# Kernel optimization log

Measured on AMD Instinct MI355X. Metric: run time of the kernel, lower is better.

## Reference

```python
import jax, jax.numpy as jnp
import numpy as np

H = 12           # num_heads
D_MODEL = 768
SCALE = (D_MODEL // H) ** -0.5  # qk_scale default: head_dim**-0.5


def _attn_mask(q, k, v, mask):
    # sim: (b, i, j); mask broadcast over query dim (mask.unsqueeze(1) in torch)
    sim = jnp.einsum('bid,bjd->bij', q, k) + mask[:, None, :]
    a = jax.nn.softmax(sim, axis=-1)
    return jnp.einsum('bij,bjd->bid', a, v)


def setup_inputs() -> dict:
    key = jax.random.key(0)
    k0, k1, k2, k3 = jax.random.split(key, 4)
    B, F, n, D = 16, 8, 196, 768
    N = 1 + F * n  # cls + frames*patches = 1569
    x = jax.random.normal(k0, (B, N, D), jnp.float32)
    x_mask = jax.random.normal(k1, (B, N), jnp.float32)  # additive attention mask
    Wqkv = jax.random.normal(k2, (3 * D, D), jnp.float32) * (D ** -0.5)
    Wproj = jax.random.normal(k3, (D, D), jnp.float32) * (D ** -0.5)
    bproj = jnp.zeros((D,), jnp.float32)
    return {"x": x, "x_mask": x_mask, "Wqkv": Wqkv, "Wproj": Wproj,
            "bproj": bproj, "f": F}


def reference(x, x_mask, Wqkv, Wproj, bproj, f):
    B, N, D = x.shape
    h = H
    d = D // h
    # qkv projection (qkv_bias=False), split into q,k,v
    qkv = x @ Wqkv.T                       # (B, N, 3D)
    q, k, v = jnp.split(qkv, 3, axis=-1)

    def to_heads(t):  # 'b n (h d) -> (b h) n d'
        return t.reshape(B, N, h, d).transpose(0, 2, 1, 3).reshape(B * h, N, d)

    q, k, v = map(to_heads, (q, k, v))
    mask = jnp.repeat(x_mask, h, axis=0)   # repeat_interleave over heads: (B*h, N)

    q = q * SCALE
    cls_q, q_ = q[:, :1], q[:, 1:]
    cls_k, k_ = k[:, :1], k[:, 1:]
    cls_v, v_ = v[:, :1], v[:, 1:]
    cls_mask, mask_ = mask[:, :1], mask[:, 1:]

    # cls token attends to everything
    cls_out = _attn_mask(cls_q, k, v, mask)            # (B*h, 1, d)

    # spatial attention: 'b (f n) d -> (b f) n d'
    n = (N - 1) // f
    q_ = q_.reshape(B * h * f, n, d)
    k_ = k_.reshape(B * h * f, n, d)
    v_ = v_.reshape(B * h * f, n, d)
    mask_ = mask_.reshape(B * h * f, n)

    # prepend cls k/v/mask to every frame group (r = f)
    cls_k = jnp.repeat(cls_k, f, axis=0)               # (B*h*f, 1, d)
    cls_v = jnp.repeat(cls_v, f, axis=0)
    cls_m = jnp.repeat(cls_mask, f, axis=0)            # (B*h*f, 1)
    k_ = jnp.concatenate([cls_k, k_], axis=1)          # (B*h*f, n+1, d)
    v_ = jnp.concatenate([cls_v, v_], axis=1)
    m2 = jnp.concatenate([cls_m, mask_], axis=1)       # (B*h*f, n+1)

    out = _attn_mask(q_, k_, v_, m2)                   # (B*h*f, n, d)
    out = out.reshape(B * h, f * n, d)                 # '(b f) n d -> b (f n) d'
    out = jnp.concatenate([cls_out, out], axis=1)      # (B*h, N, d)
    out = out.reshape(B, h, N, d).transpose(0, 2, 1, 3).reshape(B, N, D)
    return out @ Wproj.T + bproj
```

## Files before the change

### kernel.cpp

```cpp
#include <hip/hip_runtime.h>
#include <hip/hip_bf16.h>
#include <stdint.h>

#define Hh 12
#define Dm 768
#define Bb 16
#define Nt 1569
#define Ff 8
#define NC 196
#define BH 192
#define Mr 25104
#define CPW 224
#define VTW (8*CPW)
#define PLD 232
#define CLD 132

typedef __attribute__((ext_vector_type(8))) short bf16x8;
typedef __attribute__((ext_vector_type(4))) float f32x4;

typedef const __attribute__((address_space(1))) uint32_t guint;
typedef __attribute__((address_space(3))) uint32_t luint;

static __device__ __forceinline__ float bf2f(unsigned short u) {
  union { unsigned int i; float f; } v; v.i = ((unsigned int)u) << 16; return v.f;
}
static __device__ __forceinline__ unsigned short f2bf(float f) {
  __hip_bfloat16 h = __float2bfloat16(f);
  return __builtin_bit_cast(unsigned short, h);
}

__global__ void cast3_k(const float4* __restrict__ s0, ushort4* __restrict__ d0, int n0,
                        const float4* __restrict__ s1, ushort4* __restrict__ d1, int n1,
                        const float4* __restrict__ s2, ushort4* __restrict__ d2, int n2) {
  int nTot = n0 + n1 + n2;
  for (int i = blockIdx.x * blockDim.x + threadIdx.x; i < nTot; i += gridDim.x * blockDim.x) {
    const float4* s; ushort4* d; int off;
    if (i < n0) { s = s0; d = d0; off = i; }
    else if (i < n0 + n1) { s = s1; d = d1; off = i - n0; }
    else { s = s2; d = d2; off = i - n0 - n1; }
    float4 f = s[off];
    ushort4 u;
    u.x = f2bf(f.x); u.y = f2bf(f.y); u.z = f2bf(f.z); u.w = f2bf(f.w);
    d[off] = u;
  }
}

template<int MODE>
__global__ __launch_bounds__(256) void gemm_k(
    const __hip_bfloat16* __restrict__ A,
    const __hip_bfloat16* __restrict__ W,
    int M, int K,
    __hip_bfloat16* __restrict__ qh, __hip_bfloat16* __restrict__ kh,
    __hip_bfloat16* __restrict__ vT, __hip_bfloat16* __restrict__ vcls,
    const float* __restrict__ bias, float* __restrict__ outp)
{
  __shared__ __align__(16) unsigned short shmem[128 * CLD];
  unsigned short* ls0 = shmem;
  unsigned short* ls1 = shmem + 4096;
  unsigned short* ls2 = shmem + 8192;
  unsigned short* ls3 = shmem + 12288;

  const int tid = threadIdx.x;
  const int lane = tid & 63, wid = tid >> 6;
  const int waveM = wid >> 1, waveN = wid & 1;

  const int gridN = gridDim.x;
  const int nwg = gridDim.x * gridDim.y;
  int bid = blockIdx.y * gridN + blockIdx.x;
  int q8 = nwg >> 3, r8 = nwg & 7;
  int xcd = bid & 7, lid = bid >> 3;
  int swz = (xcd < r8 ? xcd * (q8 + 1) : r8 * (q8 + 1) + (xcd - r8) * q8) + lid;
  const int mBase = (swz / gridN) * 128, nBase = (swz % gridN) * 128;

  const int l15 = lane & 15, lg = lane >> 4;
  f32x4 acc[4][4] = {};
  const int nkt = K >> 6;
  for (int kt = 0; kt < nkt; ++kt) {
#pragma unroll
    for (int s = 0; s < 2; ++s) {
      int seg = s * 256 + tid;
      int row = seg >> 2, ks = seg & 3;
      int arow = mBase + row; if (arow >= M) arow = M - 1;
      int brow = nBase + row;
      const __hip_bfloat16* ap = A + (size_t)arow * K + kt * 64 + ks * 8;
      const __hip_bfloat16* wp = W + (size_t)brow * K + kt * 64 + ks * 8;
      __builtin_amdgcn_global_load_lds((guint*)ap,        (luint*)&ls0[seg * 8], 16, 0, 0);
      __builtin_amdgcn_global_load_lds((guint*)wp,        (luint*)&ls1[seg * 8], 16, 0, 0);
      __builtin_amdgcn_global_load_lds((guint*)(ap + 32), (luint*)&ls2[seg * 8], 16, 0, 0);
      __builtin_amdgcn_global_load_lds((guint*)(wp + 32), (luint*)&ls3[seg * 8], 16, 0, 0);
    }
    __syncthreads();
    bf16x8 aF[4], bF[4], aG[4], bG[4];
#pragma unroll
    for (int i = 0; i < 4; ++i) {
      int ro = (waveM * 64 + i * 16 + l15) * 32 + lg * 8;
      int co = (waveN * 64 + i * 16 + l15) * 32 + lg * 8;
      aF[i] = *reinterpret_cast<const bf16x8*>(&ls0[ro]);
      bF[i] = *reinterpret_cast<const bf16x8*>(&ls1[co]);
      aG[i] = *reinterpret_cast<const bf16x8*>(&ls2[ro]);
      bG[i] = *reinterpret_cast<const bf16x8*>(&ls3[co]);
    }
#pragma unroll
    for (int mi = 0; mi < 4; ++mi)
#pragma unroll
      for (int ni = 0; ni < 4; ++ni) {
        acc[mi][ni] = __builtin_amdgcn_mfma_f32_16x16x32_bf16(aF[mi], bF[ni], acc[mi][ni], 0, 0, 0);
        acc[mi][ni] = __builtin_amdgcn_mfma_f32_16x16x32_bf16(aG[mi], bG[ni], acc[mi][ni], 0, 0, 0);
      }
    __syncthreads();
  }

  if (MODE == 1) {
    const bool fullM = (mBase + 128 <= M);
#pragma unroll
    for (int mi = 0; mi < 4; ++mi)
#pragma unroll
      for (int ni = 0; ni < 4; ++ni)
#pragma unroll
        for (int r = 0; r < 4; ++r) {
          int grow = mBase + waveM * 64 + mi * 16 + lg * 4 + r;
          if (!fullM && grow >= M) continue;
          int gcol = nBase + waveN * 64 + ni * 16 + l15;
          outp[(size_t)grow * Dm + gcol] = acc[mi][ni][r] + bias[gcol];
        }
    return;
  }

  const int which = nBase / Dm;
  const int headBase = (nBase - which * Dm) >> 6;
  const float scl = (which == 0) ? 0.125f : 1.f;
  const bool fullM = (mBase + 128 <= M);

  if (fullM) {
    if (which < 2) {
#pragma unroll
      for (int mi = 0; mi < 4; ++mi)
#pragma unroll
        for (int ni = 0; ni < 4; ++ni)
#pragma unroll
          for (int r = 0; r < 4; ++r)
            shmem[(waveM * 64 + mi * 16 + lg * 4 + r) * CLD + (waveN * 64 + ni * 16 + l15)]
                = f2bf(acc[mi][ni][r] * scl);
      __syncthreads();
      __hip_bfloat16* dst = (which == 0) ? qh : kh;
      int row = tid >> 1, h = tid & 1;
      int grow = mBase + row;
      int b = grow / Nt, i = grow - b * Nt;
      const uint2* sp = reinterpret_cast<const uint2*>(&shmem[row * CLD + h * 64]);
      uint2* dp = reinterpret_cast<uint2*>(
          dst + ((size_t)(b * Hh + headBase + h) * Nt + i) * 64);
#pragma unroll
      for (int j = 0; j < 16; ++j) dp[j] = sp[j];
    } else {
#pragma unroll
      for (int mi = 0; mi < 4; ++mi)
#pragma unroll
        for (int ni = 0; ni < 4; ++ni)
#pragma unroll
          for (int r = 0; r < 4; ++r)
            shmem[(waveN * 64 + ni * 16 + l15) * CLD + (waveM * 64 + mi * 16 + lg * 4 + r)]
                = f2bf(acc[mi][ni][r]);
      __syncthreads();
      int lc = tid & 127, rhalf = tid >> 7;
      int h = lc >> 6, dc = lc & 63;
      int head = headBase + h;
#pragma unroll
      for (int g = 0; g < 8; ++g) {
        int row0 = rhalf * 64 + g * 8;
        int grow0 = mBase + row0;
        int b = grow0 / Nt, i0 = grow0 - b * Nt;
        const unsigned short* sp = &shmem[lc * CLD + row0];
        if (i0 >= 1 && i0 + 8 <= Nt) {
          int j0 = i0 - 1, cc = j0 / NC, key = j0 - cc * NC;
          if (key + 8 <= NC) {
            int bh = b * Hh + head;
            __hip_bfloat16* p = vT + ((size_t)bh * 64 + dc) * VTW + cc * CPW + key;
            if ((key & 1) == 0) {
              const unsigned int* s4 = reinterpret_cast<const unsigned int*>(sp);
              unsigned int* d4 = reinterpret_cast<unsigned int*>(p);
              d4[0] = s4[0]; d4[1] = s4[1]; d4[2] = s4[2]; d4[3] = s4[3];
            } else {
#pragma unroll
              for (int j = 0; j < 8; ++j)
                p[j] = __builtin_bit_cast(__hip_bfloat16, sp[j]);
            }
            continue;
          }
        }
#pragma unroll
        for (int j = 0; j < 8; ++j) {
          int grow = grow0 + j;
          int bb = grow / Nt, ii = grow - bb * Nt;
          int bh2 = bb * Hh + head;
          unsigned short val = sp[j];
          if (ii == 0) {
            vcls[bh2 * 64 + dc] = __builtin_bit_cast(__hip_bfloat16, val);
          } else {
            int jj = ii - 1, cc2 = jj / NC, k2 = jj - cc2 * NC;
            vT[((size_t)bh2 * 64 + dc) * VTW + cc2 * CPW + k2]
                = __builtin_bit_cast(__hip_bfloat16, val);
          }
        }
      }
    }
  } else {
#pragma unroll
    for (int mi = 0; mi < 4; ++mi)
#pragma unroll
      for (int ni = 0; ni < 4; ++ni)
#pragma unroll
        for (int r = 0; r < 4; ++r) {
          int grow = mBase + waveM * 64 + mi * 16 + lg * 4 + r;
          if (grow >= M) continue;
          int gcol = nBase + waveN * 64 + ni * 16 + l15;
          float v = acc[mi][ni][r];
          int b = grow / Nt, i = grow - b * Nt;
          int hcol = gcol - which * Dm;
          int head = hcol >> 6, dc = hcol & 63;
          int bh = b * Hh + head;
          if (which == 0) {
            qh[((size_t)bh * Nt + i) * 64 + dc] = __float2bfloat16(v * 0.125f);
          } else if (which == 1) {
            kh[((size_t)bh * Nt + i) * 64 + dc] = __float2bfloat16(v);
          } else {
            if (i == 0) vcls[bh * 64 + dc] = __float2bfloat16(v);
            else {
              int j = i - 1; int cc = j / NC, key = j - cc * NC;
              vT[((size_t)bh * 64 + dc) * VTW + cc * CPW + key] = __float2bfloat16(v);
            }
          }
        }
  }
}

__global__ __launch_bounds__(512, 2) void attn_k(
    const __hip_bfloat16* __restrict__ qh, const __hip_bfloat16* __restrict__ kh,
    const __hip_bfloat16* __restrict__ vT, const __hip_bfloat16* __restrict__ vcls,
    const float* __restrict__ x_mask, __hip_bfloat16* __restrict__ ao)
{
  __shared__ __align__(16) char smem[118784];

  const int bidx = blockIdx.x;
  const int tid = threadIdx.x;

  if (bidx < BH) {
    float* sS = reinterpret_cast<float*>(smem);
    float* qv = reinterpret_cast<float*>(smem + 6400);
    float* red = reinterpret_cast<float*>(smem + 6656);
    const int bh = bidx, b = bh / Hh, head = bh - b * Hh;
    if (tid < 64) qv[tid] = __bfloat162float(qh[((size_t)bh * Nt) * 64 + tid]);
    __syncthreads();
    float lmax = -1e30f;
    for (int j = tid; j < Nt; j += 512) {
      const __hip_bfloat16* kr = kh + ((size_t)bh * Nt + j) * 64;
      float dot = 0.f;
#pragma unroll
      for (int d0 = 0; d0 < 64; d0 += 8) {
        bf16x8 kv = *reinterpret_cast<const bf16x8*>(kr + d0);
#pragma unroll
        for (int i = 0; i < 8; ++i) dot += qv[d0 + i] * bf2f((unsigned short)kv[i]);
      }
      float s = dot + x_mask[b * Nt + j];
      sS[j] = s;
      lmax = fmaxf(lmax, s);
    }
    red[tid] = lmax; __syncthreads();
    for (int off = 256; off > 0; off >>= 1) {
      if (tid < off) red[tid] = fmaxf(red[tid], red[tid + off]);
      __syncthreads();
    }
    float m = red[0]; __syncthreads();
    float lsum = 0.f;
    for (int j = tid; j < Nt; j += 512) { float e = __expf(sS[j] - m); sS[j] = e; lsum += e; }
    red[tid] = lsum; __syncthreads();
    for (int off = 256; off > 0; off >>= 1) {
      if (tid < off) red[tid] += red[tid + off];
      __syncthreads();
    }
    float rden = 1.f / red[0]; __syncthreads();
    int dc = tid & 63, part = tid >> 6;
    float partial = 0.f;
    if (part == 0) partial = sS[0] * __bfloat162float(vcls[bh * 64 + dc]);
    {
      int base = 1 + part * NC;
      const __hip_bfloat16* vc2 = vT + ((size_t)bh * 64 + dc) * VTW + part * CPW;
      int key = 0;
      for (; key + 8 <= NC; key += 8) {
        bf16x8 vv = *reinterpret_cast<const bf16x8*>(vc2 + key);
#pragma unroll
        for (int i = 0; i < 8; ++i)
          partial += sS[base + key + i] * bf2f((unsigned short)vv[i]);
      }
      for (; key < NC; ++key)
        partial += sS[base + key] * __bfloat162float(vc2[key]);
    }
    red[tid] = partial; __syncthreads();
    if (tid < 64) {
      float o = 0.f;
#pragma unroll
      for (int k = 0; k < 8; ++k) o += red[tid + 64 * k];
      ao[((size_t)b * Nt) * Dm + head * 64 + dc] = __float2bfloat16(o * rden);
    }
    return;
  }

  __hip_bfloat16* ldsK = reinterpret_cast<__hip_bfloat16*>(smem);
  __hip_bfloat16* ldsV = reinterpret_cast<__hip_bfloat16*>(smem + 26624);
  __hip_bfloat16* ldsP = reinterpret_cast<__hip_bfloat16*>(smem + 59392);

  const int g = bidx - BH;
  const int bh = g >> 3, c = g & 7;
  const int b = bh / Hh, head = bh - b * Hh;
  const int lane = tid & 63, wid = tid >> 6;
  const int l15 = lane & 15, lg = lane >> 4;

  const int kbase = 1 + c * NC;

#pragma unroll
  for (int it = 0; it < 4; ++it) {
    int idx = it * 512 + tid;
    if (idx < 1664) {
      int row = idx >> 3, c16 = idx & 7;
      int token = kbase + row; if (token > Nt - 1) token = Nt - 1;
      __builtin_amdgcn_global_load_lds(
          (guint*)(kh + ((size_t)bh * Nt + token) * 64 + ((c16 ^ (row & 7)) * 8)),
          (luint*)&ldsK[idx * 8], 16, 0, 0);
    }
  }
#pragma unroll
  for (int it = 0; it < 4; ++it) {
    int idx = it * 512 + tid;
    if (idx < 1792) {
      int dc = idx / 28, u = idx - dc * 28;
      uint4 v = *reinterpret_cast<const uint4*>(
          vT + ((size_t)bh * 64 + dc) * VTW + c * CPW + u * 8);
      *reinterpret_cast<uint4*>(&ldsV[dc * 256 + ((u ^ (dc & 7)) * 8)]) = v;
    }
  }
  __syncthreads();

  __hip_bfloat16* myP = ldsP + wid * (16 * PLD);

  const __hip_bfloat16* kc = kh + (size_t)bh * Nt * 64;
  bf16x8 ck0 = *reinterpret_cast<const bf16x8*>(kc + lg * 8);
  bf16x8 ck1 = *reinterpret_cast<const bf16x8*>(kc + 32 + lg * 8);
  const float maskCls = x_mask[b * Nt];

  for (int rt = wid; rt < 13; rt += 8) {
    int qlrow = rt * 16 + l15;
    int qtok = 1 + c * NC + qlrow; if (qtok > Nt - 1) qtok = Nt - 1;
    const __hip_bfloat16* qp = qh + ((size_t)bh * Nt + qtok) * 64;
    bf16x8 aQ0 = *reinterpret_cast<const bf16x8*>(qp + lg * 8);
    bf16x8 aQ1 = *reinterpret_cast<const bf16x8*>(qp + 32 + lg * 8);

    float pc0 = 0.f;
#pragma unroll
    for (int i = 0; i < 8; ++i)
      pc0 += bf2f((unsigned short)aQ0[i]) * bf2f((unsigned short)ck0[i])
           + bf2f((unsigned short)aQ1[i]) * bf2f((unsigned short)ck1[i]);
    pc0 += __shfl_xor(pc0, 16);
    pc0 += __shfl_xor(pc0, 32);
    pc0 += maskCls;

    f32x4 S[13];
    float mv[13];
#define LD_MM(i) { \
    int row = (i) * 16 + l15; \
    bf16x8 kb0 = *reinterpret_cast<const bf16x8*>(&ldsK[row * 64 + ((lg ^ (l15 & 7)) * 8)]); \
    bf16x8 kb1 = *reinterpret_cast<const bf16x8*>(&ldsK[row * 64 + (((4 + lg) ^ (l15 & 7)) * 8)]); \
    mv[i] = (row < NC) ? x_mask[b * Nt + kbase + row] : -1e30f; \
    f32x4 sa = {}; \
    sa = __builtin_amdgcn_mfma_f32_16x16x32_bf16(aQ0, kb0, sa, 0, 0, 0); \
    sa = __builtin_amdgcn_mfma_f32_16x16x32_bf16(aQ1, kb1, sa, 0, 0, 0); \
    S[i][0] = sa[0] + mv[i]; S[i][1] = sa[1] + mv[i]; \
    S[i][2] = sa[2] + mv[i]; S[i][3] = sa[3] + mv[i]; }
    LD_MM(0) LD_MM(1) LD_MM(2) LD_MM(3) LD_MM(4) LD_MM(5) LD_MM(6)
    LD_MM(7) LD_MM(8) LD_MM(9) LD_MM(10) LD_MM(11) LD_MM(12)
#undef LD_MM

    float pcls[4], rden[4];
#pragma unroll
    for (int r = 0; r < 4; ++r) {
      float m = -1e30f;
#pragma unroll
      for (int nt = 0; nt < 13; ++nt) m = fmaxf(m, S[nt][r]);
      m = fmaxf(m, __shfl_xor(m, 1));
      m = fmaxf(m, __shfl_xor(m, 2));
      m = fmaxf(m, __shfl_xor(m, 4));
      m = fmaxf(m, __shfl_xor(m, 8));
      float sc = __shfl(pc0, lg * 4 + r);
      m = fmaxf(m, sc);
      float sum = 0.f;
#pragma unroll
      for (int nt = 0; nt < 13; ++nt) { float e = __expf(S[nt][r] - m); S[nt][r] = e; sum += e; }
      sum += __shfl_xor(sum, 1);
      sum += __shfl_xor(sum, 2);
      sum += __shfl_xor(sum, 4);
      sum += __shfl_xor(sum, 8);
      float pc = __expf(sc - m);
      pcls[r] = pc;
      rden[r] = 1.f / (sum + pc);
    }

#pragma unroll
    for (int nt = 0; nt < 13; ++nt)
#pragma unroll
      for (int r = 0; r < 4; ++r)
        myP[(lg * 4 + r) * PLD + nt * 16 + l15] = __float2bfloat16(S[nt][r]);
#pragma unroll
    for (int r = 0; r < 4; ++r)
      myP[l15 * PLD + 208 + lg * 4 + r] = __float2bfloat16(0.f);
    asm volatile("s_waitcnt lgkmcnt(0)" ::: "memory");
    __builtin_amdgcn_sched_barrier(0);

    f32x4 O[4] = {};
#define PVK(kt) { \
    bf16x8 aP = *reinterpret_cast<const bf16x8*>(&myP[l15 * PLD + (kt) * 32 + lg * 8]); \
    { int dc = 0 * 16 + l15; bf16x8 bV = *reinterpret_cast<const bf16x8*>(&ldsV[dc * 256 + ((((kt) * 4 + lg) ^ (l15 & 7)) * 8)]); \
      O[0] = __builtin_amdgcn_mfma_f32_16x16x32_bf16(aP, bV, O[0], 0, 0, 0); } \
    { int dc = 1 * 16 + l15; bf16x8 bV = *reinterpret_cast<const bf16x8*>(&ldsV[dc * 256 + ((((kt) * 4 + lg) ^ (l15 & 7)) * 8)]); \
      O[1] = __builtin_amdgcn_mfma_f32_16x16x32_bf16(aP, bV, O[1], 0, 0, 0); } \
    { int dc = 2 * 16 + l15; bf16x8 bV = *reinterpret_cast<const bf16x8*>(&ldsV[dc * 256 + ((((kt) * 4 + lg) ^ (l15 & 7)) * 8)]); \
      O[2] = __builtin_amdgcn_mfma_f32_16x16x32_bf16(aP, bV, O[2], 0, 0, 0); } \
    { int dc = 3 * 16 + l15; bf16x8 bV = *reinterpret_cast<const bf16x8*>(&ldsV[dc * 256 + ((((kt) * 4 + lg) ^ (l15 & 7)) * 8)]); \
      O[3] = __builtin_amdgcn_mfma_f32_16x16x32_bf16(aP, bV, O[3], 0, 0, 0); } }
    PVK(0) PVK(1) PVK(2) PVK(3) PVK(4) PVK(5) PVK(6)
#undef PVK

#pragma unroll
    for (int ni = 0; ni < 4; ++ni) {
      int dc = ni * 16 + l15;
      float vc = __bfloat162float(vcls[bh * 64 + dc]);
#pragma unroll
      for (int r = 0; r < 4; ++r) {
        int lrow = rt * 16 + lg * 4 + r;
        if (lrow < NC) {
          float o = (O[ni][r] + pcls[r] * vc) * rden[r];
          int tok = 1 + c * NC + lrow;
          ao[((size_t)b * Nt + tok) * Dm + head * 64 + dc] = __float2bfloat16(o);
        }
      }
    }
  }
}

extern "C" void kernel_launch(void* const* d_in, const int* in_sizes, int n_in,
                              void* d_out, int out_size, void* d_ws, size_t ws_size,
                              hipStream_t stream) {
  const float* x     = (const float*)d_in[0];
  const float* xmask = (const float*)d_in[1];
  const float* wqkv  = (const float*)d_in[2];
  const float* wproj = (const float*)d_in[3];
  const float* bproj = (const float*)d_in[4];
  float* outp = (float*)d_out;

  char* ws = (char*)d_ws;
  size_t off = 0;
  auto alloc = [&](size_t bytes) {
    char* p = ws + off;
    off += (bytes + 255) & ~(size_t)255;
    return p;
  };
  __hip_bfloat16* xb     = (__hip_bfloat16*)alloc((size_t)Mr * Dm * 2);
  __hip_bfloat16* wqkvb  = (__hip_bfloat16*)alloc((size_t)3 * Dm * Dm * 2);
  __hip_bfloat16* wprojb = (__hip_bfloat16*)alloc((size_t)Dm * Dm * 2);
  __hip_bfloat16* qh     = (__hip_bfloat16*)alloc((size_t)BH * Nt * 64 * 2);
  __hip_bfloat16* kh     = (__hip_bfloat16*)alloc((size_t)BH * Nt * 64 * 2);
  __hip_bfloat16* vT     = (__hip_bfloat16*)alloc((size_t)BH * 64 * VTW * 2);
  __hip_bfloat16* vcls   = (__hip_bfloat16*)alloc((size_t)BH * 64 * 2);
  __hip_bfloat16* ao = xb;

  cast3_k<<<2048, 256, 0, stream>>>((const float4*)x, (ushort4*)xb, Mr * Dm / 4,
                                    (const float4*)wqkv, (ushort4*)wqkvb, 3 * Dm * Dm / 4,
                                    (const float4*)wproj, (ushort4*)wprojb, Dm * Dm / 4);

  gemm_k<0><<<dim3(18, 197), 256, 0, stream>>>(xb, wqkvb, Mr, Dm, qh, kh, vT, vcls, nullptr, nullptr);

  attn_k<<<BH + BH * Ff, 512, 0, stream>>>(qh, kh, vT, vcls, xmask, ao);

  gemm_k<1><<<dim3(6, 197), 256, 0, stream>>>(ao, wprojb, Mr, Dm, nullptr, nullptr, nullptr, nullptr, bproj, outp);
}
```

Before: 300.2 us.

## Widen GEMM tiles to 128x256 with 512 threads and raise MFMA wave priority

```diff
diff --git a/kernel.cpp b/kernel.cpp
--- a/kernel.cpp
+++ b/kernel.cpp
@@ -46,7 +46,7 @@
 }
 
 template<int MODE>
-__global__ __launch_bounds__(256) void gemm_k(
+__global__ __launch_bounds__(512) void gemm_k(
     const __hip_bfloat16* __restrict__ A,
     const __hip_bfloat16* __restrict__ W,
     int M, int K,
@@ -54,15 +54,16 @@
     __hip_bfloat16* __restrict__ vT, __hip_bfloat16* __restrict__ vcls,
     const float* __restrict__ bias, float* __restrict__ outp)
 {
-  __shared__ __align__(16) unsigned short shmem[128 * CLD];
-  unsigned short* ls0 = shmem;
-  unsigned short* ls1 = shmem + 4096;
-  unsigned short* ls2 = shmem + 8192;
-  unsigned short* ls3 = shmem + 12288;
+  __shared__ __align__(16) unsigned short shmem[24576];
+  unsigned short* lsA0 = shmem;
+  unsigned short* lsA1 = shmem + 4096;
+  unsigned short* lsB0 = shmem + 8192;
+  unsigned short* lsB1 = shmem + 16384;
 
   const int tid = threadIdx.x;
   const int lane = tid & 63, wid = tid >> 6;
-  const int waveM = wid >> 1, waveN = wid & 1;
+  const int wm = wid >> 2, wn = wid & 3;
+  const int l15 = lane & 15, lg = lane >> 4;
 
   const int gridN = gridDim.x;
   const int nwg = gridDim.x * gridDim.y;
@@ -70,35 +71,36 @@
   int q8 = nwg >> 3, r8 = nwg & 7;
   int xcd = bid & 7, lid = bid >> 3;
   int swz = (xcd < r8 ? xcd * (q8 + 1) : r8 * (q8 + 1) + (xcd - r8) * q8) + lid;
-  const int mBase = (swz / gridN) * 128, nBase = (swz % gridN) * 128;
-
-  const int l15 = lane & 15, lg = lane >> 4;
+  const int mBase = (swz / gridN) * 128, nBase = (swz % gridN) * 256;
+
   f32x4 acc[4][4] = {};
   const int nkt = K >> 6;
   for (int kt = 0; kt < nkt; ++kt) {
-#pragma unroll
-    for (int s = 0; s < 2; ++s) {
-      int seg = s * 256 + tid;
-      int row = seg >> 2, ks = seg & 3;
+    {
+      int row = tid >> 2, ks = tid & 3;
       int arow = mBase + row; if (arow >= M) arow = M - 1;
-      int brow = nBase + row;
       const __hip_bfloat16* ap = A + (size_t)arow * K + kt * 64 + ks * 8;
-      const __hip_bfloat16* wp = W + (size_t)brow * K + kt * 64 + ks * 8;
-      __builtin_amdgcn_global_load_lds((guint*)ap,        (luint*)&ls0[seg * 8], 16, 0, 0);
-      __builtin_amdgcn_global_load_lds((guint*)wp,        (luint*)&ls1[seg * 8], 16, 0, 0);
-      __builtin_amdgcn_global_load_lds((guint*)(ap + 32), (luint*)&ls2[seg * 8], 16, 0, 0);
-      __builtin_amdgcn_global_load_lds((guint*)(wp + 32), (luint*)&ls3[seg * 8], 16, 0, 0);
+      __builtin_amdgcn_global_load_lds((guint*)ap,        (luint*)&lsA0[tid * 8], 16, 0, 0);
+      __builtin_amdgcn_global_load_lds((guint*)(ap + 32), (luint*)&lsA1[tid * 8], 16, 0, 0);
+#pragma unroll
+      for (int s = 0; s < 2; ++s) {
+        int idx = s * 512 + tid;
+        int brow = nBase + (idx >> 2), ks2 = idx & 3;
+        const __hip_bfloat16* wp = W + (size_t)brow * K + kt * 64 + ks2 * 8;
+        __builtin_amdgcn_global_load_lds((guint*)wp,        (luint*)&lsB0[idx * 8], 16, 0, 0);
+        __builtin_amdgcn_global_load_lds((guint*)(wp + 32), (luint*)&lsB1[idx * 8], 16, 0, 0);
+      }
     }
     __syncthreads();
     bf16x8 aF[4], bF[4], aG[4], bG[4];
 #pragma unroll
     for (int i = 0; i < 4; ++i) {
-      int ro = (waveM * 64 + i * 16 + l15) * 32 + lg * 8;
-      int co = (waveN * 64 + i * 16 + l15) * 32 + lg * 8;
-      aF[i] = *reinterpret_cast<const bf16x8*>(&ls0[ro]);
-      bF[i] = *reinterpret_cast<const bf16x8*>(&ls1[co]);
-      aG[i] = *reinterpret_cast<const bf16x8*>(&ls2[ro]);
-      bG[i] = *reinterpret_cast<const bf16x8*>(&ls3[co]);
+      int ro = (wm * 64 + i * 16 + l15) * 32 + lg * 8;
+      int co = (wn * 64 + i * 16 + l15) * 32 + lg * 8;
+      aF[i] = *reinterpret_cast<const bf16x8*>(&lsA0[ro]);
+      bF[i] = *reinterpret_cast<const bf16x8*>(&lsB0[co]);
+      aG[i] = *reinterpret_cast<const bf16x8*>(&lsA1[ro]);
+      bG[i] = *reinterpret_cast<const bf16x8*>(&lsB1[co]);
     }
 #pragma unroll
     for (int mi = 0; mi < 4; ++mi)
@@ -118,9 +120,9 @@
       for (int ni = 0; ni < 4; ++ni)
 #pragma unroll
         for (int r = 0; r < 4; ++r) {
-          int grow = mBase + waveM * 64 + mi * 16 + lg * 4 + r;
+          int grow = mBase + wm * 64 + mi * 16 + lg * 4 + r;
           if (!fullM && grow >= M) continue;
-          int gcol = nBase + waveN * 64 + ni * 16 + l15;
+          int gcol = nBase + wn * 64 + ni * 16 + l15;
           outp[(size_t)grow * Dm + gcol] = acc[mi][ni][r] + bias[gcol];
         }
     return;
@@ -133,74 +135,88 @@
 
   if (fullM) {
     if (which < 2) {
-#pragma unroll
-      for (int mi = 0; mi < 4; ++mi)
-#pragma unroll
-        for (int ni = 0; ni < 4; ++ni)
-#pragma unroll
-          for (int r = 0; r < 4; ++r)
-            shmem[(waveM * 64 + mi * 16 + lg * 4 + r) * CLD + (waveN * 64 + ni * 16 + l15)]
-                = f2bf(acc[mi][ni][r] * scl);
-      __syncthreads();
       __hip_bfloat16* dst = (which == 0) ? qh : kh;
-      int row = tid >> 1, h = tid & 1;
-      int grow = mBase + row;
-      int b = grow / Nt, i = grow - b * Nt;
-      const uint2* sp = reinterpret_cast<const uint2*>(&shmem[row * CLD + h * 64]);
-      uint2* dp = reinterpret_cast<uint2*>(
-          dst + ((size_t)(b * Hh + headBase + h) * Nt + i) * 64);
-#pragma unroll
-      for (int j = 0; j < 16; ++j) dp[j] = sp[j];
+#pragma unroll
+      for (int ch = 0; ch < 2; ++ch) {
+        if (ch) __syncthreads();
+        if ((wn >> 1) == ch) {
+#pragma unroll
+          for (int mi = 0; mi < 4; ++mi)
+#pragma unroll
+            for (int ni = 0; ni < 4; ++ni)
+#pragma unroll
+              for (int r = 0; r < 4; ++r)
+                shmem[(wm * 64 + mi * 16 + lg * 4 + r) * CLD + ((wn & 1) * 64 + ni * 16 + l15)]
+                    = f2bf(acc[mi][ni][r] * scl);
+        }
+        __syncthreads();
+        int row = tid >> 2, part = tid & 3;
+        int h2 = part >> 1, seg = part & 1;
+        int grow = mBase + row;
+        int b = grow / Nt, i = grow - b * Nt;
+        int hsel = headBase + ch * 2 + h2;
+        const uint2* sp = reinterpret_cast<const uint2*>(&shmem[row * CLD + h2 * 64 + seg * 32]);
+        uint2* dp = reinterpret_cast<uint2*>(
+            dst + ((size_t)(b * Hh + hsel) * Nt + i) * 64 + seg * 32);
+#pragma unroll
+        for (int j = 0; j < 8; ++j) dp[j] = sp[j];
+      }
     } else {
 #pragma unroll
-      for (int mi = 0; mi < 4; ++mi)
-#pragma unroll
-        for (int ni = 0; ni < 4; ++ni)
-#pragma unroll
-          for (int r = 0; r < 4; ++r)
-            shmem[(waveN * 64 + ni * 16 + l15) * CLD + (waveM * 64 + mi * 16 + lg * 4 + r)]
-                = f2bf(acc[mi][ni][r]);
-      __syncthreads();
-      int lc = tid & 127, rhalf = tid >> 7;
-      int h = lc >> 6, dc = lc & 63;
-      int head = headBase + h;
-#pragma unroll
-      for (int g = 0; g < 8; ++g) {
-        int row0 = rhalf * 64 + g * 8;
-        int grow0 = mBase + row0;
-        int b = grow0 / Nt, i0 = grow0 - b * Nt;
-        const unsigned short* sp = &shmem[lc * CLD + row0];
-        if (i0 >= 1 && i0 + 8 <= Nt) {
-          int j0 = i0 - 1, cc = j0 / NC, key = j0 - cc * NC;
-          if (key + 8 <= NC) {
-            int bh = b * Hh + head;
-            __hip_bfloat16* p = vT + ((size_t)bh * 64 + dc) * VTW + cc * CPW + key;
-            if ((key & 1) == 0) {
-              const unsigned int* s4 = reinterpret_cast<const unsigned int*>(sp);
-              unsigned int* d4 = reinterpret_cast<unsigned int*>(p);
-              d4[0] = s4[0]; d4[1] = s4[1]; d4[2] = s4[2]; d4[3] = s4[3];
+      for (int ch = 0; ch < 2; ++ch) {
+        if (ch) __syncthreads();
+        if ((wn >> 1) == ch) {
+#pragma unroll
+          for (int mi = 0; mi < 4; ++mi)
+#pragma unroll
+            for (int ni = 0; ni < 4; ++ni)
+#pragma unroll
+              for (int r = 0; r < 4; ++r)
+                shmem[((wn & 1) * 64 + ni * 16 + l15) * CLD + (wm * 64 + mi * 16 + lg * 4 + r)]
+                    = f2bf(acc[mi][ni][r]);
+        }
+        __syncthreads();
+        int lc = tid & 127, rblk = tid >> 7;
+        int colg = ch * 128 + lc;
+        int head = headBase + (colg >> 6), dc = colg & 63;
+#pragma unroll
+        for (int gi = 0; gi < 4; ++gi) {
+          int row0 = rblk * 32 + gi * 8;
+          int grow0 = mBase + row0;
+          int b = grow0 / Nt, i0 = grow0 - b * Nt;
+          const unsigned short* sp = &shmem[lc * CLD + row0];
+          if (i0 >= 1 && i0 + 8 <= Nt) {
+            int j0 = i0 - 1, cc = j0 / NC, key = j0 - cc * NC;
+            if (key + 8 <= NC) {
+              int bh = b * Hh + head;
+              __hip_bfloat16* p = vT + ((size_t)bh * 64 + dc) * VTW + cc * CPW + key;
+              if ((key & 1) == 0) {
+                const unsigned int* s4 = reinterpret_cast<const unsigned int*>(sp);
+                unsigned int* d4 = reinterpret_cast<unsigned int*>(p);
+                d4[0] = s4[0]; d4[1] = s4[1]; d4[2] = s4[2]; d4[3] = s4[3];
+              } else {
+#pragma unroll
+                for (int j = 0; j < 8; ++j)
+                  p[j] = __builtin_bit_cast(__hip_bfloat16, sp[j]);
+              }
+              continue;
+            }
+          }
+#pragma unroll
+          for (int j = 0; j < 8; ++j) {
+            int grow = grow0 + j;
+            int bb = grow / Nt, ii = grow - bb * Nt;
+            int bh2 = bb * Hh + head;
+            unsigned short val = sp[j];
+            if (ii == 0) {
+              vcls[bh2 * 64 + dc] = __builtin_bit_cast(__hip_bfloat16, val);
             } else {
-#pragma unroll
-              for (int j = 0; j < 8; ++j)
-                p[j] = __builtin_bit_cast(__hip_bfloat16, sp[j]);
+              int jj = ii - 1, cc2 = jj / NC, k2 = jj - cc2 * NC;
+              vT[((size_t)bh2 * 64 + dc) * VTW + cc2 * CPW + k2]
+                  = __builtin_bit_cast(__hip_bfloat16, val);
             }
-            continue;
           }
         }
-#pragma unroll
-        for (int j = 0; j < 8; ++j) {
-          int grow = grow0 + j;
-          int bb = grow / Nt, ii = grow - bb * Nt;
-          int bh2 = bb * Hh + head;
-          unsigned short val = sp[j];
-          if (ii == 0) {
-            vcls[bh2 * 64 + dc] = __builtin_bit_cast(__hip_bfloat16, val);
-          } else {
-            int jj = ii - 1, cc2 = jj / NC, k2 = jj - cc2 * NC;
-            vT[((size_t)bh2 * 64 + dc) * VTW + cc2 * CPW + k2]
-                = __builtin_bit_cast(__hip_bfloat16, val);
-          }
-        }
       }
     }
   } else {
@@ -210,9 +226,9 @@
       for (int ni = 0; ni < 4; ++ni)
 #pragma unroll
         for (int r = 0; r < 4; ++r) {
-          int grow = mBase + waveM * 64 + mi * 16 + lg * 4 + r;
+          int grow = mBase + wm * 64 + mi * 16 + lg * 4 + r;
           if (grow >= M) continue;
-          int gcol = nBase + waveN * 64 + ni * 16 + l15;
+          int gcol = nBase + wn * 64 + ni * 16 + l15;
           float v = acc[mi][ni][r];
           int b = grow / Nt, i = grow - b * Nt;
           int hcol = gcol - which * Dm;
@@ -364,6 +380,7 @@
 
     f32x4 S[13];
     float mv[13];
+    __builtin_amdgcn_s_setprio(1);
 #define LD_MM(i) { \
     int row = (i) * 16 + l15; \
     bf16x8 kb0 = *reinterpret_cast<const bf16x8*>(&ldsK[row * 64 + ((lg ^ (l15 & 7)) * 8)]); \
@@ -377,6 +394,7 @@
     LD_MM(0) LD_MM(1) LD_MM(2) LD_MM(3) LD_MM(4) LD_MM(5) LD_MM(6)
     LD_MM(7) LD_MM(8) LD_MM(9) LD_MM(10) LD_MM(11) LD_MM(12)
 #undef LD_MM
+    __builtin_amdgcn_s_setprio(0);
 
     float pcls[4], rden[4];
 #pragma unroll
@@ -414,6 +432,7 @@
     __builtin_amdgcn_sched_barrier(0);
 
     f32x4 O[4] = {};
+    __builtin_amdgcn_s_setprio(1);
 #define PVK(kt) { \
     bf16x8 aP = *reinterpret_cast<const bf16x8*>(&myP[l15 * PLD + (kt) * 32 + lg * 8]); \
     { int dc = 0 * 16 + l15; bf16x8 bV = *reinterpret_cast<const bf16x8*>(&ldsV[dc * 256 + ((((kt) * 4 + lg) ^ (l15 & 7)) * 8)]); \
@@ -426,6 +445,7 @@
       O[3] = __builtin_amdgcn_mfma_f32_16x16x32_bf16(aP, bV, O[3], 0, 0, 0); } }
     PVK(0) PVK(1) PVK(2) PVK(3) PVK(4) PVK(5) PVK(6)
 #undef PVK
+    __builtin_amdgcn_s_setprio(0);
 
 #pragma unroll
     for (int ni = 0; ni < 4; ++ni) {
@@ -474,9 +494,9 @@
                                     (const float4*)wqkv, (ushort4*)wqkvb, 3 * Dm * Dm / 4,
                                     (const float4*)wproj, (ushort4*)wprojb, Dm * Dm / 4);
 
-  gemm_k<0><<<dim3(18, 197), 256, 0, stream>>>(xb, wqkvb, Mr, Dm, qh, kh, vT, vcls, nullptr, nullptr);
+  gemm_k<0><<<dim3(9, 197), 512, 0, stream>>>(xb, wqkvb, Mr, Dm, qh, kh, vT, vcls, nullptr, nullptr);
 
   attn_k<<<BH + BH * Ff, 512, 0, stream>>>(qh, kh, vT, vcls, xmask, ao);
 
-  gemm_k<1><<<dim3(6, 197), 256, 0, stream>>>(ao, wprojb, Mr, Dm, nullptr, nullptr, nullptr, nullptr, bproj, outp);
+  gemm_k<1><<<dim3(3, 197), 512, 0, stream>>>(ao, wprojb, Mr, Dm, nullptr, nullptr, nullptr, nullptr, bproj, outp);
 }
```

Result: slower. 340.8 us (+13.5%).
